# Kernel tuning notes

Measured on AMD Instinct MI355X. Metric: run time of the kernel, lower is better.

Reference implementation:

```python
import jax, jax.numpy as jnp
import numpy as np

SAMPLES = 16        # samples per spatial dim -> M = SAMPLES**2 sample points
SAMPLE_PAD = 0
K = 9               # nearest neighbors == conv kernel size == stride


def setup_inputs() -> dict:
    key = jax.random.key(0)
    k1, k2, k3 = jax.random.split(key, 3)
    B, C, H, W = 16, 128, 64, 64
    OUT = 128
    x = jax.random.normal(k1, (B, C, H, W), dtype=jnp.float32)
    w = jax.random.normal(k2, (OUT, C, K), dtype=jnp.float32) * 0.05
    b = jax.random.normal(k3, (OUT,), dtype=jnp.float32) * 0.05
    return {"x": x, "w": w, "b": b}


def reference(x, w, b):
    B, C, H, W = x.shape
    N = H * W
    # --- spatial sample grid (static, shape-derived) ---
    xi = jnp.round(jnp.linspace(SAMPLE_PAD, H - SAMPLE_PAD - 1, SAMPLES)).astype(jnp.int32)
    yi = jnp.round(jnp.linspace(SAMPLE_PAD, W - SAMPLE_PAD - 1, SAMPLES)).astype(jnp.int32)
    xg, yg = jnp.meshgrid(xi, yi, indexing='ij')
    x_sample = x[:, :, xg, yg].reshape(B, C, -1)          # (B, C, M)
    x1 = x.reshape(B, C, N)                                # (B, C, N)
    # --- squared Euclidean distance between tokens and samples ---
    dots = jnp.einsum('bcn,bcm->bnm', x1, x_sample)        # (B, N, M)
    n2 = jnp.sum(x1 * x1, axis=1)                          # (B, N)
    m2 = jnp.sum(x_sample * x_sample, axis=1)              # (B, M)
    dist2 = n2[:, :, None] + m2[:, None, :] - 2.0 * dots   # (B, N, M)
    # K nearest samples per token (smallest distance)
    _, idx = jax.lax.top_k(-dist2, K)                      # (B, N, K) int32
    # gather neighbor features from the sample set: (B, C, N, K)
    nbrs = jnp.take_along_axis(x_sample[:, :, None, :],
                               idx[:, None, :, :], axis=3)
    # Conv1d(kernel=K, stride=K) over the (B, C, N*K) prime tensor
    out = jnp.einsum('bcnk,ock->bon', nbrs, w) + b[None, :, None]
    return out.reshape(B, w.shape[0], H, W)
```

## Files before the change

### kernel.cpp

```cpp
#include <hip/hip_runtime.h>

#define NB   16
#define NC   128
#define NN   4096
#define NM   256
#define NK   9
#define NO   128

typedef __attribute__((ext_vector_type(8))) short bf16x8;
typedef __attribute__((ext_vector_type(4))) float f32x4;

__device__ __constant__ int d_grid16[16] = {0,4,8,13,17,21,25,29,34,38,42,46,50,55,59,63};

__device__ inline unsigned short bf16_rne(float v) {
    unsigned u = __float_as_uint(v);
    return (unsigned short)((u + 0x7FFFu + ((u >> 16) & 1u)) >> 16);
}

__device__ inline void merge16(unsigned* s, const unsigned* q) {
    unsigned r[16];
    #pragma unroll
    for (int i = 0; i < 16; ++i) r[i] = min(s[i], q[15 - i]);
    #pragma unroll
    for (int d = 8; d >= 1; d >>= 1)
        #pragma unroll
        for (int i = 0; i < 16; ++i)
            if (!(i & d)) { unsigned a = r[i], b2 = r[i + d]; r[i] = min(a, b2); r[i + d] = max(a, b2); }
    #pragma unroll
    for (int i = 0; i < 16; ++i) s[i] = r[i];
}

__global__ __launch_bounds__(256) void k_prep(const float* __restrict__ x,
                                              const float* __restrict__ w,
                                              float* __restrict__ xsT,
                                              unsigned short* __restrict__ xsTh,
                                              unsigned short* __restrict__ xsTl,
                                              unsigned short* __restrict__ Wth,
                                              unsigned short* __restrict__ Wtl,
                                              float* __restrict__ n2g,
                                              float* __restrict__ m2) {
    __shared__ float tile[16 * 260];
    int bx = blockIdx.x, t = threadIdx.x;
    if (bx < 128) {
        int b = bx >> 3, c0 = (bx & 7) * 16;
        int m = t;
        int pix = d_grid16[m >> 4] * 64 + d_grid16[m & 15];
        #pragma unroll
        for (int cc = 0; cc < 16; ++cc)
            tile[cc * 260 + m] = x[((size_t)b * NC + c0 + cc) * NN + pix];
        __syncthreads();
        #pragma unroll
        for (int e = 0; e < 4; ++e) {
            float fv[4];
            fv[0] = tile[(4 * e + 0) * 260 + m];
            fv[1] = tile[(4 * e + 1) * 260 + m];
            fv[2] = tile[(4 * e + 2) * 260 + m];
            fv[3] = tile[(4 * e + 3) * 260 + m];
            size_t base = ((size_t)b * NM + m) * NC + c0 + 4 * e;
            *(float4*)&xsT[base] = make_float4(fv[0], fv[1], fv[2], fv[3]);
            unsigned short h4[4], l4[4];
            #pragma unroll
            for (int e2 = 0; e2 < 4; ++e2) {
                unsigned short h = bf16_rne(fv[e2]);
                h4[e2] = h;
                l4[e2] = bf16_rne(fv[e2] - __uint_as_float(((unsigned)h) << 16));
            }
            *(ushort4*)&xsTh[base] = make_ushort4(h4[0], h4[1], h4[2], h4[3]);
            *(ushort4*)&xsTl[base] = make_ushort4(l4[0], l4[1], l4[2], l4[3]);
        }
    } else if (bx < 704) {
        int f = (bx - 128) * 256 + t;
        int ko = f >> 7, c = f & 127;
        int o = ko & 127, k = ko >> 7;
        float v = w[(size_t)o * 1152 + c * 9 + k];
        unsigned short h = bf16_rne(v);
        Wth[f] = h;
        Wtl[f] = bf16_rne(v - __uint_as_float(((unsigned)h) << 16));
    } else if (bx < 960) {
        #pragma clang fp contract(off)
        int i = bx - 704;
        int b = i >> 4, n = (i & 15) * 256 + t;
        const float* p = x + (size_t)b * NC * NN + n;
        float a = 0.f;
        #pragma unroll 16
        for (int c = 0; c < NC; ++c) { float v = p[(size_t)c * NN]; a = __fadd_rn(a, __fmul_rn(v, v)); }
        n2g[(size_t)b * NN + n] = a;
    } else {
        #pragma clang fp contract(off)
        int b = bx - 960;
        int pix = d_grid16[t >> 4] * 64 + d_grid16[t & 15];
        const float* p = x + (size_t)b * NC * NN + pix;
        float a = 0.f;
        #pragma unroll 16
        for (int c = 0; c < NC; ++c) { float v = p[(size_t)c * NN]; a = __fadd_rn(a, __fmul_rn(v, v)); }
        m2[b * NM + t] = a;
    }
}

__global__ __launch_bounds__(256) void k_g(const unsigned short* __restrict__ xsTh,
                                           const unsigned short* __restrict__ xsTl,
                                           const unsigned short* __restrict__ Wth,
                                           const unsigned short* __restrict__ Wtl,
                                           float* __restrict__ G) {
    int id = blockIdx.x;
    int b = id & 15, r = id >> 4;
    int kk = r % 9, q = r / 9;
    int mt = q >> 1, jh = q & 1;
    int t = threadIdx.x;
    int w = t >> 6, lane = t & 63;
    int lr = lane & 15, quad = lane >> 4;
    int m = b * NM + mt * 64 + w * 16 + lr;
    const unsigned short* aph = xsTh + (size_t)m * NC;
    const unsigned short* apl = xsTl + (size_t)m * NC;
    f32x4 acc[4];
    #pragma unroll
    for (int j = 0; j < 4; ++j) acc[j] = (f32x4){0.f, 0.f, 0.f, 0.f};
    #pragma unroll
    for (int kb = 0; kb < 4; ++kb) {
        int co = kb * 32 + quad * 8;
        bf16x8 Ah = *(const bf16x8*)&aph[co];
        bf16x8 Al = *(const bf16x8*)&apl[co];
        #pragma unroll
        for (int j = 0; j < 4; ++j) {
            size_t wrow = ((size_t)kk * 128 + jh * 64 + 16 * j + lr) * NC + co;
            bf16x8 Bh = *(const bf16x8*)&Wth[wrow];
            bf16x8 Bl = *(const bf16x8*)&Wtl[wrow];
            acc[j] = __builtin_amdgcn_mfma_f32_16x16x32_bf16(Ah, Bh, acc[j], 0, 0, 0);
            acc[j] = __builtin_amdgcn_mfma_f32_16x16x32_bf16(Al, Bh, acc[j], 0, 0, 0);
            acc[j] = __builtin_amdgcn_mfma_f32_16x16x32_bf16(Ah, Bl, acc[j], 0, 0, 0);
        }
    }
    int mrow = b * NM + mt * 64 + w * 16 + quad * 4;
    #pragma unroll
    for (int j = 0; j < 4; ++j)
        #pragma unroll
        for (int r2 = 0; r2 < 4; ++r2)
            G[((size_t)(mrow + r2)) * 1152 + kk * 128 + jh * 64 + 16 * j + lr] = acc[j][r2];
}

__global__ __launch_bounds__(256, 2) void k_sel(const float* __restrict__ x,
                                                const unsigned short* __restrict__ xsTh,
                                                const unsigned short* __restrict__ xsTl,
                                                const float* __restrict__ m2,
                                                int* __restrict__ idx) {
    __shared__ __align__(16) unsigned short xhp[32 * 136];
    __shared__ __align__(16) unsigned short xlp[32 * 136];
    __shared__ __align__(16) unsigned wl[2 * 4 * 16 * 16];
    __shared__ float m2l[256];

    int b = blockIdx.x & 15, n0 = (blockIdx.x >> 4) * 32;
    int t = threadIdx.x;
    int w = t >> 6, lane = t & 63;
    int lr = lane & 15, quad = lane >> 4;

    m2l[t] = m2[b * NM + t];

    #pragma unroll
    for (int it = 0; it < 4; ++it) {
        int f4 = it * 256 + t;
        int c = f4 >> 3, nn4 = (f4 & 7) * 4;
        float4 v = *(const float4*)&x[((size_t)b * NC + c) * NN + n0 + nn4];
        float vf[4] = {v.x, v.y, v.z, v.w};
        #pragma unroll
        for (int e = 0; e < 4; ++e) {
            unsigned short h = bf16_rne(vf[e]);
            unsigned short l = bf16_rne(vf[e] - __uint_as_float(((unsigned)h) << 16));
            xhp[(nn4 + e) * 136 + c] = h;
            xlp[(nn4 + e) * 136 + c] = l;
        }
    }
    __syncthreads();

    f32x4 acc[2][4];
    #pragma unroll
    for (int i = 0; i < 2; ++i)
        #pragma unroll
        for (int j = 0; j < 4; ++j) acc[i][j] = (f32x4){0.f, 0.f, 0.f, 0.f};
    int mbase = w * 64;
    #pragma unroll
    for (int kb = 0; kb < 4; ++kb) {
        int co = kb * 32 + quad * 8;
        bf16x8 Bh0 = *(const bf16x8*)&xhp[lr * 136 + co];
        bf16x8 Bl0 = *(const bf16x8*)&xlp[lr * 136 + co];
        bf16x8 Bh1 = *(const bf16x8*)&xhp[(16 + lr) * 136 + co];
        bf16x8 Bl1 = *(const bf16x8*)&xlp[(16 + lr) * 136 + co];
        bf16x8 Ah[4], Al[4];
        #pragma unroll
        for (int j = 0; j < 4; ++j) {
            size_t arow = ((size_t)(b * NM + mbase + 16 * j + lr)) * NC + co;
            Ah[j] = *(const bf16x8*)&xsTh[arow];
            Al[j] = *(const bf16x8*)&xsTl[arow];
        }
        #pragma unroll
        for (int j = 0; j < 4; ++j) {
            acc[0][j] = __builtin_amdgcn_mfma_f32_16x16x32_bf16(Ah[j], Bh0, acc[0][j], 0, 0, 0);
            acc[0][j] = __builtin_amdgcn_mfma_f32_16x16x32_bf16(Ah[j], Bl0, acc[0][j], 0, 0, 0);
            acc[0][j] = __builtin_amdgcn_mfma_f32_16x16x32_bf16(Al[j], Bh0, acc[0][j], 0, 0, 0);
            acc[1][j] = __builtin_amdgcn_mfma_f32_16x16x32_bf16(Ah[j], Bh1, acc[1][j], 0, 0, 0);
            acc[1][j] = __builtin_amdgcn_mfma_f32_16x16x32_bf16(Ah[j], Bl1, acc[1][j], 0, 0, 0);
            acc[1][j] = __builtin_amdgcn_mfma_f32_16x16x32_bf16(Al[j], Bh1, acc[1][j], 0, 0, 0);
        }
    }

    unsigned s16v[16];
    int hfirst = 1 - (w & 1);
    #pragma unroll
    for (int hh = 0; hh < 2; ++hh) {
        int h = (hh == 0) ? hfirst : 1 - hfirst;
        #pragma unroll
        for (int j = 0; j < 4; ++j)
            #pragma unroll
            for (int r = 0; r < 4; ++r) {
                int m = mbase + 16 * j + quad * 4 + r;
                float key = fmaf(-2.f, acc[h][j][r], m2l[m]);
                unsigned u = __float_as_uint(key);
                u = (u & 0x80000000u) ? ~u : (u | 0x80000000u);
                s16v[4 * j + r] = (u & 0xFFFFFF00u) | (unsigned)m;
            }
        #define CE(i,jx) { unsigned a_ = s16v[i], b_ = s16v[jx]; s16v[i] = min(a_, b_); s16v[jx] = max(a_, b_); }
        CE(0,1) CE(2,3) CE(0,2) CE(1,3) CE(1,2)
        CE(4,5) CE(6,7) CE(4,6) CE(5,7) CE(5,6)
        CE(0,4) CE(2,6) CE(2,4) CE(1,5) CE(3,7) CE(3,5) CE(1,2) CE(3,4) CE(5,6)
        CE(8,9) CE(10,11) CE(8,10) CE(9,11) CE(9,10)
        CE(12,13) CE(14,15) CE(12,14) CE(13,15) CE(13,14)
        CE(8,12) CE(10,14) CE(10,12) CE(9,13) CE(11,15) CE(11,13) CE(9,10) CE(11,12) CE(13,14)
        CE(0,8) CE(4,12) CE(4,8) CE(2,10) CE(6,14) CE(6,10) CE(2,4) CE(6,8) CE(10,12)
        CE(1,9) CE(5,13) CE(5,9) CE(3,11) CE(7,15) CE(7,11) CE(3,5) CE(7,9) CE(11,13)
        CE(1,2) CE(3,4) CE(5,6) CE(7,8) CE(9,10) CE(11,12) CE(13,14)
        #undef CE

        #pragma unroll
        for (int d = 16; d <= 32; d <<= 1) {
            unsigned q[16];
            #pragma unroll
            for (int i = 0; i < 16; ++i) q[i] = (unsigned)__shfl_xor((int)s16v[i], d, 64);
            merge16(s16v, q);
        }
        if (quad == 0) {
            #pragma unroll
            for (int ii = 0; ii < 4; ++ii)
                *(uint4*)&wl[(((h * 4 + w) * 16 + lr) * 16) + 4 * ii] =
                    make_uint4(s16v[4*ii], s16v[4*ii+1], s16v[4*ii+2], s16v[4*ii+3]);
        }
    }
    __syncthreads();

    if (w < 2) {
        int h = w;
        #pragma unroll
        for (int p = 1; p < 4; ++p) {
            int pw = (w + p) & 3;
            unsigned q[16];
            #pragma unroll
            for (int i = 0; i < 16; ++i) q[i] = wl[(((h * 4 + pw) * 16 + lr) * 16) + i];
            merge16(s16v, q);
        }
        if (quad == 0) {
            int tok = 16 * h + lr;
            size_t obase = (size_t)(b * NN + n0 + tok) * NK;
            #pragma unroll
            for (int i = 0; i < 4; ++i)
                idx[obase + i] = (int)((s16v[4*i] & 255u) | ((s16v[4*i+1] & 255u) << 8) |
                                       ((s16v[4*i+2] & 255u) << 16) | ((s16v[4*i+3] & 255u) << 24));
        }
    }
}

__global__ __launch_bounds__(256, 2) void k_ref(const float* __restrict__ x,
                                                const float* __restrict__ xsT,
                                                const float* __restrict__ m2,
                                                const float* __restrict__ n2g,
                                                int* __restrict__ idx) {
    #pragma clang fp contract(off)
    __shared__ __align__(16) float xr[32 * 132];
    __shared__ unsigned long long pairs[32 * 17];
    __shared__ unsigned char candl[512];
    __shared__ float m2l[256];
    __shared__ float n2l[32];

    int b = blockIdx.x & 15, n0 = (blockIdx.x >> 4) * 32;
    int t = threadIdx.x;

    m2l[t] = m2[b * NM + t];
    if (t < 32) n2l[t] = n2g[(size_t)b * NN + n0 + t];
    if (t < 128) ((unsigned*)candl)[t] =
        (unsigned)idx[(size_t)(b * NN + n0 + (t >> 2)) * NK + (t & 3)];

    #pragma unroll
    for (int it = 0; it < 4; ++it) {
        int f4 = it * 256 + t;
        int c = f4 >> 3, nn4 = (f4 & 7) * 4;
        float4 v = *(const float4*)&x[((size_t)b * NC + c) * NN + n0 + nn4];
        xr[(nn4 + 0) * 132 + c] = v.x;
        xr[(nn4 + 1) * 132 + c] = v.y;
        xr[(nn4 + 2) * 132 + c] = v.z;
        xr[(nn4 + 3) * 132 + c] = v.w;
    }
    __syncthreads();

    int tok = t >> 3, q8 = t & 7;
    float n2 = n2l[tok];
    int mym[2];
    unsigned long long myp[2];
    #pragma unroll
    for (int s = 0; s < 2; ++s) {
        int m = candl[tok * 16 + q8 + 8 * s];
        mym[s] = m;
        const float* xt = xsT + ((size_t)(b * NM + m)) * NC;
        float dot = 0.f;
        for (int c4 = 0; c4 < 32; ++c4) {
            float4 xv = *(const float4*)&xr[tok * 132 + 4 * c4];
            float4 sv = *(const float4*)&xt[4 * c4];
            dot = __fadd_rn(dot, __fmul_rn(xv.x, sv.x));
            dot = __fadd_rn(dot, __fmul_rn(xv.y, sv.y));
            dot = __fadd_rn(dot, __fmul_rn(xv.z, sv.z));
            dot = __fadd_rn(dot, __fmul_rn(xv.w, sv.w));
        }
        float key = __fsub_rn(__fadd_rn(n2, m2l[m]), __fmul_rn(2.f, dot));
        unsigned u = __float_as_uint(key);
        u = (u & 0x80000000u) ? ~u : (u | 0x80000000u);
        myp[s] = ((unsigned long long)u << 32) | (unsigned)m;
        pairs[tok * 17 + q8 + 8 * s] = myp[s];
    }
    __syncthreads();
    unsigned long long pl[16];
    #pragma unroll
    for (int l2 = 0; l2 < 16; ++l2) pl[l2] = pairs[tok * 17 + l2];
    size_t obase = (size_t)(b * NN + n0 + tok) * NK;
    #pragma unroll
    for (int s = 0; s < 2; ++s) {
        int rank = 0;
        #pragma unroll
        for (int l2 = 0; l2 < 16; ++l2) rank += (pl[l2] < myp[s]);
        if (rank < 9) idx[obase + rank] = mym[s];
    }
}

__global__ __launch_bounds__(256) void k_out(const float* __restrict__ G,
                                             const int* __restrict__ idx,
                                             const float* __restrict__ bias,
                                             float* __restrict__ out) {
    __shared__ float S[64 * 129];
    __shared__ int   idxl[576];
    __shared__ float biasl[128];
    int b = blockIdx.x & 15, n0 = (blockIdx.x >> 4) * 64;
    int t = threadIdx.x;
    if (t < 128) biasl[t] = bias[t];
    for (int f = t; f < 576; f += 256) idxl[f] = idx[(size_t)(b * NN + n0) * NK + f];
    __syncthreads();
    int o = t & 127, half = t >> 7;
    for (int p = 0; p < 32; ++p) {
        int n = p * 2 + half;
        float a = biasl[o];
        #pragma unroll
        for (int k = 0; k < 9; ++k) {
            int m = idxl[n * 9 + k];
            a += G[(((size_t)(b * NM + m)) * NK + k) * 128 + o];
        }
        S[n * 129 + o] = a;
    }
    __syncthreads();
    int nn = t & 63, ob = t >> 6;
    for (int p = 0; p < 32; ++p) {
        int o2 = p * 4 + ob;
        out[((size_t)(b * NO + o2)) * NN + n0 + nn] = S[nn * 129 + o2];
    }
}

extern "C" void kernel_launch(void* const* d_in, const int* in_sizes, int n_in,
                              void* d_out, int out_size, void* d_ws, size_t ws_size,
                              hipStream_t stream) {
    const float* x    = (const float*)d_in[0];
    const float* w    = (const float*)d_in[1];
    const float* bias = (const float*)d_in[2];
    float* out = (float*)d_out;

    float* ws   = (float*)d_ws;
    float* m2   = ws;
    float* n2g  = ws + 4096;
    float* xsT  = ws + 69632;
    float* G    = ws + 593920;
    int*   idx  = (int*)(ws + 5312512);
    unsigned short* xsTh = (unsigned short*)(ws + 5902336);
    unsigned short* xsTl = (unsigned short*)(ws + 6164480);
    unsigned short* Wth  = (unsigned short*)(ws + 6426624);
    unsigned short* Wtl  = (unsigned short*)(ws + 6500352);

    k_prep<<<dim3(976),  dim3(256), 0, stream>>>(x, w, xsT, xsTh, xsTl, Wth, Wtl, n2g, m2);
    k_g   <<<dim3(1152), dim3(256), 0, stream>>>(xsTh, xsTl, Wth, Wtl, G);
    k_sel <<<dim3(2048), dim3(256), 0, stream>>>(x, xsTh, xsTl, m2, idx);
    k_ref <<<dim3(2048), dim3(256), 0, stream>>>(x, xsT, m2, n2g, idx);
    k_out <<<dim3(1024), dim3(256), 0, stream>>>(G, idx, bias, out);
}
```

Baseline: 260.7 us.

## Fuse candidate refinement kernel into output gather kernel

Merges the exact-fp32 refinement of the 16 bf16-selected candidates into the output kernel, so the top-9 indices stay in shared memory instead of being written to global memory and read back. This removes one kernel launch and the global idx round trip. Each block now handles 64 tokens with 4 candidates per thread, and the transposed-x tile shares an LDS buffer with the output staging tile. The cost is more LDS per block and a serial refine-then-gather phase inside one block, which may lower occupancy.

After: 266.3 us. 2.2% more time.

```diff
diff --git a/kernel.cpp b/kernel.cpp
--- a/kernel.cpp
+++ b/kernel.cpp
@@ -17,7 +17,7 @@
     return (unsigned short)((u + 0x7FFFu + ((u >> 16) & 1u)) >> 16);
 }
 
-__device__ inline void merge16(unsigned* s, const unsigned* q) {
+__device__ __forceinline__ void merge16(unsigned* s, const unsigned* q) {
     unsigned r[16];
     #pragma unroll
     for (int i = 0; i < 16; ++i) r[i] = min(s[i], q[15 - i]);
@@ -266,30 +266,38 @@
     }
 }
 
-__global__ __launch_bounds__(256, 2) void k_ref(const float* __restrict__ x,
-                                                const float* __restrict__ xsT,
-                                                const float* __restrict__ m2,
-                                                const float* __restrict__ n2g,
-                                                int* __restrict__ idx) {
+__global__ __launch_bounds__(256) void k_out(const float* __restrict__ x,
+                                             const float* __restrict__ xsT,
+                                             const float* __restrict__ m2,
+                                             const float* __restrict__ n2g,
+                                             const float* __restrict__ G,
+                                             const int* __restrict__ idx,
+                                             const float* __restrict__ bias,
+                                             float* __restrict__ out) {
     #pragma clang fp contract(off)
-    __shared__ __align__(16) float xr[32 * 132];
-    __shared__ unsigned long long pairs[32 * 17];
-    __shared__ unsigned char candl[512];
+    __shared__ __align__(16) unsigned char ubuf[33792];
+    __shared__ unsigned long long pairs[64 * 17];
+    __shared__ int   idxl[576];
     __shared__ float m2l[256];
-    __shared__ float n2l[32];
-
-    int b = blockIdx.x & 15, n0 = (blockIdx.x >> 4) * 32;
+    __shared__ float n2l[64];
+    __shared__ float biasl[128];
+    float* xr = (float*)ubuf;
+    float* S  = (float*)ubuf;
+
+    int b = blockIdx.x & 15, n0 = (blockIdx.x >> 4) * 64;
     int t = threadIdx.x;
 
     m2l[t] = m2[b * NM + t];
-    if (t < 32) n2l[t] = n2g[(size_t)b * NN + n0 + t];
-    if (t < 128) ((unsigned*)candl)[t] =
-        (unsigned)idx[(size_t)(b * NN + n0 + (t >> 2)) * NK + (t & 3)];
-
-    #pragma unroll
-    for (int it = 0; it < 4; ++it) {
+    if (t < 64)  n2l[t] = n2g[(size_t)b * NN + n0 + t];
+    if (t < 128) biasl[t] = bias[t];
+
+    int tok = t >> 2, grp = t & 3;
+    unsigned candw = (unsigned)idx[(size_t)(b * NN + n0 + tok) * NK + grp];
+
+    #pragma unroll
+    for (int it = 0; it < 8; ++it) {
         int f4 = it * 256 + t;
-        int c = f4 >> 3, nn4 = (f4 & 7) * 4;
+        int c = f4 >> 4, nn4 = (f4 & 15) * 4;
         float4 v = *(const float4*)&x[((size_t)b * NC + c) * NN + n0 + nn4];
         xr[(nn4 + 0) * 132 + c] = v.x;
         xr[(nn4 + 1) * 132 + c] = v.y;
@@ -298,72 +306,65 @@
     }
     __syncthreads();
 
-    int tok = t >> 3, q8 = t & 7;
-    float n2 = n2l[tok];
-    int mym[2];
-    unsigned long long myp[2];
-    #pragma unroll
-    for (int s = 0; s < 2; ++s) {
-        int m = candl[tok * 16 + q8 + 8 * s];
-        mym[s] = m;
-        const float* xt = xsT + ((size_t)(b * NM + m)) * NC;
-        float dot = 0.f;
-        for (int c4 = 0; c4 < 32; ++c4) {
-            float4 xv = *(const float4*)&xr[tok * 132 + 4 * c4];
-            float4 sv = *(const float4*)&xt[4 * c4];
-            dot = __fadd_rn(dot, __fmul_rn(xv.x, sv.x));
-            dot = __fadd_rn(dot, __fmul_rn(xv.y, sv.y));
-            dot = __fadd_rn(dot, __fmul_rn(xv.z, sv.z));
-            dot = __fadd_rn(dot, __fmul_rn(xv.w, sv.w));
-        }
-        float key = __fsub_rn(__fadd_rn(n2, m2l[m]), __fmul_rn(2.f, dot));
-        unsigned u = __float_as_uint(key);
-        u = (u & 0x80000000u) ? ~u : (u | 0x80000000u);
-        myp[s] = ((unsigned long long)u << 32) | (unsigned)m;
-        pairs[tok * 17 + q8 + 8 * s] = myp[s];
-    }
-    __syncthreads();
-    unsigned long long pl[16];
-    #pragma unroll
-    for (int l2 = 0; l2 < 16; ++l2) pl[l2] = pairs[tok * 17 + l2];
-    size_t obase = (size_t)(b * NN + n0 + tok) * NK;
-    #pragma unroll
-    for (int s = 0; s < 2; ++s) {
-        int rank = 0;
-        #pragma unroll
-        for (int l2 = 0; l2 < 16; ++l2) rank += (pl[l2] < myp[s]);
-        if (rank < 9) idx[obase + rank] = mym[s];
-    }
-}
-
-__global__ __launch_bounds__(256) void k_out(const float* __restrict__ G,
-                                             const int* __restrict__ idx,
-                                             const float* __restrict__ bias,
-                                             float* __restrict__ out) {
-    __shared__ float S[64 * 129];
-    __shared__ int   idxl[576];
-    __shared__ float biasl[128];
-    int b = blockIdx.x & 15, n0 = (blockIdx.x >> 4) * 64;
-    int t = threadIdx.x;
-    if (t < 128) biasl[t] = bias[t];
-    for (int f = t; f < 576; f += 256) idxl[f] = idx[(size_t)(b * NN + n0) * NK + f];
-    __syncthreads();
-    int o = t & 127, half = t >> 7;
-    for (int p = 0; p < 32; ++p) {
-        int n = p * 2 + half;
-        float a = biasl[o];
-        #pragma unroll
-        for (int k = 0; k < 9; ++k) {
-            int m = idxl[n * 9 + k];
-            a += G[(((size_t)(b * NM + m)) * NK + k) * 128 + o];
-        }
-        S[n * 129 + o] = a;
-    }
-    __syncthreads();
-    int nn = t & 63, ob = t >> 6;
-    for (int p = 0; p < 32; ++p) {
-        int o2 = p * 4 + ob;
-        out[((size_t)(b * NO + o2)) * NN + n0 + nn] = S[nn * 129 + o2];
+    {
+        float n2 = n2l[tok];
+        int mym[4];
+        unsigned long long myp[4];
+        #pragma unroll
+        for (int s = 0; s < 4; ++s) {
+            int m = (int)((candw >> (8 * s)) & 255u);
+            mym[s] = m;
+            const float* xt = xsT + ((size_t)(b * NM + m)) * NC;
+            float dot = 0.f;
+            for (int c4 = 0; c4 < 32; ++c4) {
+                float4 xv = *(const float4*)&xr[tok * 132 + 4 * c4];
+                float4 sv = *(const float4*)&xt[4 * c4];
+                dot = __fadd_rn(dot, __fmul_rn(xv.x, sv.x));
+                dot = __fadd_rn(dot, __fmul_rn(xv.y, sv.y));
+                dot = __fadd_rn(dot, __fmul_rn(xv.z, sv.z));
+                dot = __fadd_rn(dot, __fmul_rn(xv.w, sv.w));
+            }
+            float key = __fsub_rn(__fadd_rn(n2, m2l[m]), __fmul_rn(2.f, dot));
+            unsigned u = __float_as_uint(key);
+            u = (u & 0x80000000u) ? ~u : (u | 0x80000000u);
+            myp[s] = ((unsigned long long)u << 32) | (unsigned)mym[s];
+            pairs[tok * 17 + grp * 4 + s] = myp[s];
+        }
+        __syncthreads();
+        unsigned long long pl[16];
+        #pragma unroll
+        for (int l2 = 0; l2 < 16; ++l2) pl[l2] = pairs[tok * 17 + l2];
+        #pragma unroll
+        for (int s = 0; s < 4; ++s) {
+            int rank = 0;
+            #pragma unroll
+            for (int l2 = 0; l2 < 16; ++l2) rank += (pl[l2] < myp[s]);
+            if (rank < 9) idxl[tok * 9 + rank] = mym[s];
+        }
+    }
+    __syncthreads();
+
+    {
+        int o = t & 127, half = t >> 7;
+        for (int p = 0; p < 32; ++p) {
+            int n = p * 2 + half;
+            float a = biasl[o];
+            #pragma unroll
+            for (int k = 0; k < 9; ++k) {
+                int m = idxl[n * 9 + k];
+                a += G[(((size_t)(b * NM + m)) * NK + k) * 128 + o];
+            }
+            S[n * 129 + o] = a;
+        }
+    }
+    __syncthreads();
+
+    {
+        int nn = t & 63, ob = t >> 6;
+        for (int p = 0; p < 32; ++p) {
+            int o2 = p * 4 + ob;
+            out[((size_t)(b * NO + o2)) * NN + n0 + nn] = S[nn * 129 + o2];
+        }
     }
 }
 
@@ -389,6 +390,5 @@
     k_prep<<<dim3(976),  dim3(256), 0, stream>>>(x, w, xsT, xsTh, xsTl, Wth, Wtl, n2g, m2);
     k_g   <<<dim3(1152), dim3(256), 0, stream>>>(xsTh, xsTl, Wth, Wtl, G);
     k_sel <<<dim3(2048), dim3(256), 0, stream>>>(x, xsTh, xsTl, m2, idx);
-    k_ref <<<dim3(2048), dim3(256), 0, stream>>>(x, xsT, m2, n2g, idx);
-    k_out <<<dim3(1024), dim3(256), 0, stream>>>(G, idx, bias, out);
-}
+    k_out <<<dim3(1024), dim3(256), 0, stream>>>(x, xsT, m2, n2g, G, idx, bias, out);
+}
```
